# Kernel optimization log

Hardware: AMD Instinct MI355X
Metric: run time of the kernel (lower is better)

The kernel has to match this reference:

```python
import jax, jax.numpy as jnp
import numpy as np

B, N, D, H, DH = 2, 2048, 1024, 16, 64
SCALE = DH ** -0.5


def setup_inputs() -> dict:
    key = jax.random.key(0)
    k1, k2, k3 = jax.random.split(key, 3)
    x = jax.random.normal(k1, (B, N, D), dtype=jnp.float32)
    w_qkv = jax.random.normal(k2, (D, 3 * H * DH), dtype=jnp.float32) * 0.02
    w_out = jax.random.normal(k3, (H * DH, D), dtype=jnp.float32) * 0.02
    # causal boolean mask, broadcast over (b, h)
    attn_mask = jnp.tril(jnp.ones((N, N), dtype=bool))
    return {"x": x, "attn_mask": attn_mask, "w_qkv": w_qkv, "w_out": w_out}


def reference(x, attn_mask, w_qkv, w_out):
    b, n, _ = x.shape
    # fused QKV projection; Rearrange 'b n (qkv h d) -> qkv b h n d'
    qkv = (x @ w_qkv).reshape(b, n, 3, H, DH)
    qkv = jnp.transpose(qkv, (2, 0, 3, 1, 4))  # [3, b, h, n, d]
    q, k, v = qkv[0], qkv[1], qkv[2]
    q = q * SCALE
    sim = jnp.einsum('bhid,bhjd->bhij', q, k)  # [b, h, n, n]
    neg = -jnp.finfo(sim.dtype).max
    sim = jnp.where(attn_mask, sim, neg)
    attn = jax.nn.softmax(sim, axis=-1)
    out = jnp.einsum('bhij,bhjd->bhid', attn, v)  # [b, h, n, d]
    out = jnp.transpose(out, (0, 2, 1, 3)).reshape(b, n, H * DH)
    return out @ w_out
```

## Files before the change

### kernel.cpp

```cpp
#include <hip/hip_runtime.h>
#include <hip/hip_bf16.h>


typedef unsigned short u16;
typedef unsigned int u32;
typedef __bf16 bf16x8 __attribute__((ext_vector_type(8)));
typedef float  f32x4  __attribute__((ext_vector_type(4)));
typedef unsigned short u16x4 __attribute__((ext_vector_type(4)));

#define DEV __device__ __forceinline__

DEV float exp2fast(float x) { return __builtin_amdgcn_exp2f(x); }

DEV u16 f2bf(float f) {
  unsigned u = __builtin_bit_cast(unsigned, f);
  return (u16)((u + 0x7FFFu + ((u >> 16) & 1u)) >> 16);
}

DEV u16 f2bf_fast(float f) {
  __bf16 h = (__bf16)f;
  return __builtin_bit_cast(u16, h);
}

DEV f32x4 mfma16(bf16x8 a, bf16x8 b, f32x4 c) {
  return __builtin_amdgcn_mfma_f32_16x16x32_bf16(a, b, c, 0, 0, 0);
}

template <typename T>
DEV void gload16(const T* g, T* l) {
  __builtin_amdgcn_global_load_lds((__attribute__((address_space(1))) void*)g,
                                   (__attribute__((address_space(3))) void*)l, 16, 0, 0);
}


__global__ __launch_bounds__(256) void prep(const float* __restrict__ x,
                                            const float* __restrict__ wq,
                                            const float* __restrict__ wo,
                                            u16* __restrict__ xb,
                                            u16* __restrict__ dq,
                                            u16* __restrict__ dow) {
  __shared__ u16 T[64][72];
  const int tid = threadIdx.x;
  const int id = (int)blockIdx.x;
  if (id < 4096) {
    int idx = (id * 256 + tid) * 4;
    float4 v = *(const float4*)(x + idx);
    u16x4 u = { f2bf(v.x), f2bf(v.y), f2bf(v.z), f2bf(v.w) };
    *(u16x4*)(xb + idx) = u;
    return;
  }
  int wid = id - 4096;
  int bx = wid & 63, by = wid >> 6;
  const float* src; u16* dst; int C, sl;
  if (bx < 48) { src = wq; dst = dq; C = 3072; sl = 1024; }
  else         { bx -= 48; src = wo; dst = dow; C = 1024; sl = 0; }
  const int c0 = bx * 64, r0 = by * 64;
  const int cl = tid & 63;
  const float scale = (c0 + cl < sl) ? 0.125f * 1.4426950408889634f : 1.0f;
#pragma unroll
  for (int i = 0; i < 16; ++i) {
    int r = (tid >> 6) * 16 + i;
    T[cl][r] = f2bf(src[(size_t)(r0 + r) * C + c0 + cl] * scale);
  }
  __syncthreads();
#pragma unroll
  for (int i = 0; i < 16; ++i) {
    int cc = (tid >> 6) * 16 + i;
    dst[(size_t)(c0 + cc) * 1024 + r0 + cl] = T[cc][cl];
  }
}


__global__ __launch_bounds__(256) void gemm_bf16(const u16* __restrict__ A,
                                                 const u16* __restrict__ Bt,
                                                 u16* __restrict__ qk,
                                                 u16* __restrict__ vt,
                                                 int nx, int cpx) {
  __shared__ __align__(16) u16 lA[128 * 64];
  __shared__ __align__(16) u16 lB[128 * 64];
  const int tid = threadIdx.x;
  const int lane = tid & 63, w = tid >> 6;
  const int g = lane >> 4, r16 = lane & 15;
  const int wm = w >> 1, wn = w & 1;
  const int id = (int)blockIdx.x;
  const int newid = (id & 7) * cpx + (id >> 3);
  const int m0 = (newid / nx) * 128, n0 = (newid % nx) * 128;

  const f32x4 z4 = {0.f, 0.f, 0.f, 0.f};
  f32x4 acc[4][4];
#pragma unroll
  for (int m = 0; m < 4; ++m)
#pragma unroll
    for (int n = 0; n < 4; ++n) acc[m][n] = z4;

  for (int kt = 0; kt < 16; ++kt) {
    const int kbase = kt * 64;
#pragma unroll
    for (int issue = 0; issue < 4; ++issue) {
      int i = issue * 256 + tid;
      int r = i >> 3, jp = (i & 7) ^ (r & 7);
      gload16(A + (size_t)(m0 + r) * 1024 + kbase + jp * 8,
              lA + (size_t)(issue * 256 + (tid & ~63)) * 8);
      gload16(Bt + (size_t)(n0 + r) * 1024 + kbase + jp * 8,
              lB + (size_t)(issue * 256 + (tid & ~63)) * 8);
    }
    __syncthreads();
#pragma unroll
    for (int kk = 0; kk < 2; ++kk) {
      bf16x8 a[4], b[4];
#pragma unroll
      for (int m = 0; m < 4; ++m) {
        int row = wm * 64 + m * 16 + r16;
        int off = row * 128 + ((kk * 64 + g * 16) ^ ((r16 & 7) << 4));
        a[m] = *(const bf16x8*)((const char*)lA + off);
      }
#pragma unroll
      for (int n = 0; n < 4; ++n) {
        int row = wn * 64 + n * 16 + r16;
        int off = row * 128 + ((kk * 64 + g * 16) ^ ((r16 & 7) << 4));
        b[n] = *(const bf16x8*)((const char*)lB + off);
      }
      __builtin_amdgcn_s_setprio(1);
#pragma unroll
      for (int m = 0; m < 4; ++m)
#pragma unroll
        for (int n = 0; n < 4; ++n) acc[m][n] = mfma16(a[m], b[n], acc[m][n]);
      __builtin_amdgcn_s_setprio(0);
    }
    __syncthreads();
  }
  if (n0 < 2048) {
#pragma unroll
    for (int m = 0; m < 4; ++m)
#pragma unroll
      for (int n = 0; n < 4; ++n) {
        int col = n0 + wn * 64 + n * 16 + r16;
#pragma unroll
        for (int j = 0; j < 4; ++j) {
          int row = m0 + wm * 64 + m * 16 + g * 4 + j;
          qk[(size_t)row * 2048 + col] = f2bf(acc[m][n][j]);
        }
      }
  } else {
#pragma unroll
    for (int m = 0; m < 4; ++m) {
      int row0 = m0 + wm * 64 + m * 16 + g * 4;
      int b = row0 >> 11, nn0 = row0 & 2047;
#pragma unroll
      for (int n = 0; n < 4; ++n) {
        int hcol = n0 - 2048 + wn * 64 + n * 16 + r16;
        int h = hcol >> 6, d = hcol & 63;
        u16x4 pk = { f2bf(acc[m][n][0]), f2bf(acc[m][n][1]),
                     f2bf(acc[m][n][2]), f2bf(acc[m][n][3]) };
        *(u16x4*)(vt + (size_t)((b * 16 + h) * 64 + d) * 2048 + nn0) = pk;
      }
    }
  }
}


__global__ __launch_bounds__(256) void gemm64(const u16* __restrict__ A,
                                              const u16* __restrict__ Bt,
                                              float* __restrict__ Cf,
                                              int N, int nx, int cpx) {
  __shared__ __align__(16) u16 lA[64 * 64];
  __shared__ __align__(16) u16 lB[64 * 64];
  const int tid = threadIdx.x;
  const int lane = tid & 63, w = tid >> 6;
  const int g = lane >> 4, r16 = lane & 15;
  const int wm = w >> 1, wn = w & 1;
  const int id = (int)blockIdx.x;
  const int newid = (id & 7) * cpx + (id >> 3);
  const int m0 = (newid / nx) * 64, n0 = (newid % nx) * 64;

  const f32x4 z4 = {0.f, 0.f, 0.f, 0.f};
  f32x4 acc[2][2];
#pragma unroll
  for (int m = 0; m < 2; ++m)
#pragma unroll
    for (int n = 0; n < 2; ++n) acc[m][n] = z4;

  for (int kt = 0; kt < 16; ++kt) {
    const int kbase = kt * 64;
#pragma unroll
    for (int issue = 0; issue < 2; ++issue) {
      int i = issue * 256 + tid;
      int r = i >> 3, jp = (i & 7) ^ (r & 7);
      gload16(A + (size_t)(m0 + r) * 1024 + kbase + jp * 8,
              lA + (size_t)(issue * 256 + (tid & ~63)) * 8);
      gload16(Bt + (size_t)(n0 + r) * 1024 + kbase + jp * 8,
              lB + (size_t)(issue * 256 + (tid & ~63)) * 8);
    }
    __syncthreads();
#pragma unroll
    for (int kk = 0; kk < 2; ++kk) {
      bf16x8 a[2], b[2];
#pragma unroll
      for (int m = 0; m < 2; ++m) {
        int row = wm * 32 + m * 16 + r16;
        int off = row * 128 + ((kk * 64 + g * 16) ^ ((r16 & 7) << 4));
        a[m] = *(const bf16x8*)((const char*)lA + off);
      }
#pragma unroll
      for (int n = 0; n < 2; ++n) {
        int row = wn * 32 + n * 16 + r16;
        int off = row * 128 + ((kk * 64 + g * 16) ^ ((r16 & 7) << 4));
        b[n] = *(const bf16x8*)((const char*)lB + off);
      }
      __builtin_amdgcn_s_setprio(1);
#pragma unroll
      for (int m = 0; m < 2; ++m)
#pragma unroll
        for (int n = 0; n < 2; ++n) acc[m][n] = mfma16(a[m], b[n], acc[m][n]);
      __builtin_amdgcn_s_setprio(0);
    }
    __syncthreads();
  }
#pragma unroll
  for (int m = 0; m < 2; ++m)
#pragma unroll
    for (int n = 0; n < 2; ++n) {
      int col = n0 + wn * 32 + n * 16 + r16;
#pragma unroll
      for (int j = 0; j < 4; ++j) {
        int row = m0 + wm * 32 + m * 16 + g * 4 + j;
        Cf[(size_t)row * N + col] = acc[m][n][j];
      }
    }
}


__global__ __launch_bounds__(256) void attn_fused(const u16* __restrict__ qk,
                                                  const u16* __restrict__ vt,
                                                  u16* __restrict__ ao) {
  __shared__ __align__(16) u16 lK[2][64 * 64];
  __shared__ __align__(16) u16 lV[2][64 * 64];
  const int tid = threadIdx.x;
  const int lane = tid & 63, w = tid >> 6;
  const int g = lane >> 4, r16 = lane & 15;

  const int flat = (int)blockIdx.x;
  const int xcd = flat & 7;
  const int cu = (flat >> 3) & 31;
  const int round = (flat >> 8) & 3;
  const int grp = xcd * 4 + round;
  const int qt = (round < 2) ? (31 - cu) : cu;
  const int b = grp >> 4, h = grp & 15;
  const int q0w = qt * 64 + w * 16;

  bf16x8 aq[2];
  {
    const u16* qrow = qk + (size_t)(b * 2048 + q0w + r16) * 2048 + h * 64;
    aq[0] = *(const bf16x8*)(qrow + g * 8);
    aq[1] = *(const bf16x8*)(qrow + 32 + g * 8);
  }

  const int r = tid >> 3, jp = (tid & 7) ^ (r & 7);
  const int rp = (r & 0x23) | ((r & 0x0C) << 1) | ((r & 0x10) >> 2);
  const u16* ksrc = qk + (size_t)(b * 2048 + rp) * 2048 + 1024 + h * 64 + jp * 8;
  const u16* vsrc = vt + (size_t)((b * 16 + h) * 64 + r) * 2048 + jp * 8;
  const size_t ldst = (size_t)(tid & ~63) * 8;

  const f32x4 z4 = {0.f, 0.f, 0.f, 0.f};
  f32x4 o[4];
#pragma unroll
  for (int n = 0; n < 4; ++n) o[n] = z4;
  float mrun = -INFINITY, lrun = 0.f;

  gload16(ksrc, lK[0] + ldst);
  gload16(ksrc + (size_t)32 * 2048, lK[0] + 2048 + ldst);
  gload16(vsrc, lV[0] + ldst);
  gload16(vsrc + (size_t)32 * 2048, lV[0] + 2048 + ldst);
  __syncthreads();

  int cur = 0;
  for (int t = 0; t <= qt; ++t) {
    if (t < qt) {
      const u16* kn = ksrc + (size_t)(t + 1) * 64 * 2048;
      const u16* vn = vsrc + (size_t)(t + 1) * 64;
      gload16(kn, lK[cur ^ 1] + ldst);
      gload16(kn + (size_t)32 * 2048, lK[cur ^ 1] + 2048 + ldst);
      gload16(vn, lV[cur ^ 1] + ldst);
      gload16(vn + (size_t)32 * 2048, lV[cur ^ 1] + 2048 + ldst);
    }
    f32x4 s[4];
#pragma unroll
    for (int f = 0; f < 4; ++f) s[f] = z4;
    __builtin_amdgcn_s_setprio(1);
#pragma unroll
    for (int kk = 0; kk < 2; ++kk) {
#pragma unroll
      for (int f = 0; f < 4; ++f) {
        int row = f * 16 + r16;
        int off = row * 128 + ((kk * 64 + g * 16) ^ ((r16 & 7) << 4));
        bf16x8 ak = *(const bf16x8*)((const char*)lK[cur] + off);
        s[f] = mfma16(ak, aq[kk], s[f]);
      }
    }
    __builtin_amdgcn_s_setprio(0);
    if (t == qt) {
      const int qrel = w * 16 + r16;
#pragma unroll
      for (int f = 0; f < 4; ++f)
#pragma unroll
        for (int j = 0; j < 4; ++j) {
          int kvt = (f >> 1) * 32 + g * 8 + (f & 1) * 4 + j;
          if (kvt > qrel) s[f][j] = -3.0e38f;
        }
    }
    float mx = fmaxf(fmaxf(fmaxf(s[0][0], s[0][1]), fmaxf(s[0][2], s[0][3])),
                     fmaxf(fmaxf(s[1][0], s[1][1]), fmaxf(s[1][2], s[1][3])));
    mx = fmaxf(mx, fmaxf(fmaxf(fmaxf(s[2][0], s[2][1]), fmaxf(s[2][2], s[2][3])),
                         fmaxf(fmaxf(s[3][0], s[3][1]), fmaxf(s[3][2], s[3][3]))));
    mx = fmaxf(mx, __shfl_xor(mx, 16));
    mx = fmaxf(mx, __shfl_xor(mx, 32));
    if (!__all(mx - mrun <= 8.0f)) {
      float mnew = fmaxf(mrun, mx);
      float corr = exp2fast(mrun - mnew);
      mrun = mnew;
      lrun *= corr;
      float cj[4];
#pragma unroll
      for (int j = 0; j < 4; ++j) cj[j] = __shfl(corr, g * 4 + j);
#pragma unroll
      for (int n = 0; n < 4; ++n)
#pragma unroll
        for (int j = 0; j < 4; ++j) o[n][j] *= cj[j];
    }
    float sm = 0.f;
#pragma unroll
    for (int f = 0; f < 4; ++f)
#pragma unroll
      for (int j = 0; j < 4; ++j) {
        s[f][j] = exp2fast(s[f][j] - mrun);
        sm += s[f][j];
      }
    lrun += sm;

    bf16x8 ap0, ap1;
#pragma unroll
    for (int j = 0; j < 4; ++j) {
      ap0[j]     = (__bf16)s[0][j];
      ap0[j + 4] = (__bf16)s[1][j];
      ap1[j]     = (__bf16)s[2][j];
      ap1[j + 4] = (__bf16)s[3][j];
    }
    __builtin_amdgcn_s_setprio(1);
#pragma unroll
    for (int n = 0; n < 4; ++n) {
      int row = n * 16 + r16;
      int off0 = row * 128 + ((g * 16) ^ ((r16 & 7) << 4));
      int off1 = row * 128 + ((64 + g * 16) ^ ((r16 & 7) << 4));
      bf16x8 bv0 = *(const bf16x8*)((const char*)lV[cur] + off0);
      o[n] = mfma16(ap0, bv0, o[n]);
      bf16x8 bv1 = *(const bf16x8*)((const char*)lV[cur] + off1);
      o[n] = mfma16(ap1, bv1, o[n]);
    }
    __builtin_amdgcn_s_setprio(0);
    __syncthreads();
    cur ^= 1;
  }
  float lt = lrun;
  lt += __shfl_xor(lt, 16);
  lt += __shfl_xor(lt, 32);
  float lj[4];
#pragma unroll
  for (int j = 0; j < 4; ++j) lj[j] = __shfl(lt, g * 4 + j);
#pragma unroll
  for (int n = 0; n < 4; ++n) {
    int col = h * 64 + n * 16 + r16;
#pragma unroll
    for (int j = 0; j < 4; ++j) {
      int row = b * 2048 + q0w + g * 4 + j;
      ao[(size_t)row * 1024 + col] = f2bf_fast(o[n][j] * (1.f / lj[j]));
    }
  }
}


extern "C" void kernel_launch(void* const* d_in, const int* in_sizes, int n_in,
                              void* d_out, int out_size, void* d_ws, size_t ws_size,
                              hipStream_t stream) {
  const float* x     = (const float*)d_in[0];
  const float* w_qkv = (const float*)d_in[2];
  const float* w_out = (const float*)d_in[3];
  float* out = (float*)d_out;

  u16* ws = (u16*)d_ws;
  u16* x_bf  = ws;
  u16* wqkvT = x_bf + (size_t)4096 * 1024;
  u16* woutT = wqkvT + (size_t)3072 * 1024;
  u16* qk    = woutT + (size_t)1024 * 1024;
  u16* vtb   = qk + (size_t)4096 * 2048;
  u16* ao    = vtb + (size_t)2048 * 2048;

  prep<<<5120, 256, 0, stream>>>(x, w_qkv, w_out, x_bf, wqkvT, woutT);
  gemm_bf16<<<768, 256, 0, stream>>>(x_bf, wqkvT, qk, vtb, 24, 96);
  attn_fused<<<1024, 256, 0, stream>>>(qk, vtb, ao);
  gemm64<<<1024, 256, 0, stream>>>(ao, woutT, out, 1024, 16, 128);
}
```

Measured before the change: 192.8 us.

## Double-buffer LDS tiles in both GEMMs and enlarge output GEMM tile to 128x64

Both the QKV GEMM and the output projection GEMM now keep two LDS buffers and issue the global loads for the next K tile before computing on the current one. This removes one barrier per iteration and hides load latency behind the MFMA work. The output GEMM also moves from 64x64 to 128x64 tiles, launched as 512 blocks instead of 1024, which improves reuse of the B tile. In exchange, LDS per block doubles (64KB for the QKV GEMM), which can cut occupancy, and the output GEMM has fewer blocks to spread across the CUs.

```diff
diff --git a/kernel.cpp b/kernel.cpp
--- a/kernel.cpp
+++ b/kernel.cpp
@@ -76,8 +76,8 @@
                                                  u16* __restrict__ qk,
                                                  u16* __restrict__ vt,
                                                  int nx, int cpx) {
-  __shared__ __align__(16) u16 lA[128 * 64];
-  __shared__ __align__(16) u16 lB[128 * 64];
+  __shared__ __align__(16) u16 lA[2][128 * 64];
+  __shared__ __align__(16) u16 lB[2][128 * 64];
   const int tid = threadIdx.x;
   const int lane = tid & 63, w = tid >> 6;
   const int g = lane >> 4, r16 = lane & 15;
@@ -86,6 +86,13 @@
   const int newid = (id & 7) * cpx + (id >> 3);
   const int m0 = (newid / nx) * 128, n0 = (newid % nx) * 128;
 
+  const int sr[4] = { tid >> 3, (256 + tid) >> 3, (512 + tid) >> 3, (768 + tid) >> 3 };
+  int sjp[4];
+#pragma unroll
+  for (int is = 0; is < 4; ++is) sjp[is] = ((is * 256 + tid) & 7) ^ (sr[is] & 7);
+  const size_t sdst[4] = { (size_t)(tid & ~63) * 8, (size_t)(256 + (tid & ~63)) * 8,
+                           (size_t)(512 + (tid & ~63)) * 8, (size_t)(768 + (tid & ~63)) * 8 };
+
   const f32x4 z4 = {0.f, 0.f, 0.f, 0.f};
   f32x4 acc[4][4];
 #pragma unroll
@@ -93,18 +100,23 @@
 #pragma unroll
     for (int n = 0; n < 4; ++n) acc[m][n] = z4;
 
+#pragma unroll
+  for (int is = 0; is < 4; ++is) {
+    gload16(A + (size_t)(m0 + sr[is]) * 1024 + sjp[is] * 8, lA[0] + sdst[is]);
+    gload16(Bt + (size_t)(n0 + sr[is]) * 1024 + sjp[is] * 8, lB[0] + sdst[is]);
+  }
+  __syncthreads();
+
+  int cur = 0;
   for (int kt = 0; kt < 16; ++kt) {
-    const int kbase = kt * 64;
-#pragma unroll
-    for (int issue = 0; issue < 4; ++issue) {
-      int i = issue * 256 + tid;
-      int r = i >> 3, jp = (i & 7) ^ (r & 7);
-      gload16(A + (size_t)(m0 + r) * 1024 + kbase + jp * 8,
-              lA + (size_t)(issue * 256 + (tid & ~63)) * 8);
-      gload16(Bt + (size_t)(n0 + r) * 1024 + kbase + jp * 8,
-              lB + (size_t)(issue * 256 + (tid & ~63)) * 8);
-    }
-    __syncthreads();
+    if (kt < 15) {
+      const int kb = (kt + 1) * 64;
+#pragma unroll
+      for (int is = 0; is < 4; ++is) {
+        gload16(A + (size_t)(m0 + sr[is]) * 1024 + kb + sjp[is] * 8, lA[cur ^ 1] + sdst[is]);
+        gload16(Bt + (size_t)(n0 + sr[is]) * 1024 + kb + sjp[is] * 8, lB[cur ^ 1] + sdst[is]);
+      }
+    }
 #pragma unroll
     for (int kk = 0; kk < 2; ++kk) {
       bf16x8 a[4], b[4];
@@ -112,13 +124,13 @@
       for (int m = 0; m < 4; ++m) {
         int row = wm * 64 + m * 16 + r16;
         int off = row * 128 + ((kk * 64 + g * 16) ^ ((r16 & 7) << 4));
-        a[m] = *(const bf16x8*)((const char*)lA + off);
+        a[m] = *(const bf16x8*)((const char*)lA[cur] + off);
       }
 #pragma unroll
       for (int n = 0; n < 4; ++n) {
         int row = wn * 64 + n * 16 + r16;
         int off = row * 128 + ((kk * 64 + g * 16) ^ ((r16 & 7) << 4));
-        b[n] = *(const bf16x8*)((const char*)lB + off);
+        b[n] = *(const bf16x8*)((const char*)lB[cur] + off);
       }
       __builtin_amdgcn_s_setprio(1);
 #pragma unroll
@@ -128,6 +140,7 @@
       __builtin_amdgcn_s_setprio(0);
     }
     __syncthreads();
+    cur ^= 1;
   }
   if (n0 < 2048) {
 #pragma unroll
@@ -159,72 +172,87 @@
 }
 
 
-__global__ __launch_bounds__(256) void gemm64(const u16* __restrict__ A,
-                                              const u16* __restrict__ Bt,
-                                              float* __restrict__ Cf,
-                                              int N, int nx, int cpx) {
-  __shared__ __align__(16) u16 lA[64 * 64];
-  __shared__ __align__(16) u16 lB[64 * 64];
+__global__ __launch_bounds__(256) void gemm_out(const u16* __restrict__ A,
+                                                const u16* __restrict__ Bt,
+                                                float* __restrict__ Cf,
+                                                int nx, int cpx) {
+  __shared__ __align__(16) u16 lA[2][128 * 64];
+  __shared__ __align__(16) u16 lB[2][64 * 64];
   const int tid = threadIdx.x;
   const int lane = tid & 63, w = tid >> 6;
   const int g = lane >> 4, r16 = lane & 15;
   const int wm = w >> 1, wn = w & 1;
   const int id = (int)blockIdx.x;
   const int newid = (id & 7) * cpx + (id >> 3);
-  const int m0 = (newid / nx) * 64, n0 = (newid % nx) * 64;
+  const int m0 = (newid / nx) * 128, n0 = (newid % nx) * 64;
+
+  const int sr[4] = { tid >> 3, (256 + tid) >> 3, (512 + tid) >> 3, (768 + tid) >> 3 };
+  int sjp[4];
+#pragma unroll
+  for (int is = 0; is < 4; ++is) sjp[is] = ((is * 256 + tid) & 7) ^ (sr[is] & 7);
+  const size_t sdst[4] = { (size_t)(tid & ~63) * 8, (size_t)(256 + (tid & ~63)) * 8,
+                           (size_t)(512 + (tid & ~63)) * 8, (size_t)(768 + (tid & ~63)) * 8 };
 
   const f32x4 z4 = {0.f, 0.f, 0.f, 0.f};
-  f32x4 acc[2][2];
-#pragma unroll
-  for (int m = 0; m < 2; ++m)
+  f32x4 acc[4][2];
+#pragma unroll
+  for (int m = 0; m < 4; ++m)
 #pragma unroll
     for (int n = 0; n < 2; ++n) acc[m][n] = z4;
 
+#pragma unroll
+  for (int is = 0; is < 4; ++is)
+    gload16(A + (size_t)(m0 + sr[is]) * 1024 + sjp[is] * 8, lA[0] + sdst[is]);
+#pragma unroll
+  for (int is = 0; is < 2; ++is)
+    gload16(Bt + (size_t)(n0 + sr[is]) * 1024 + sjp[is] * 8, lB[0] + sdst[is]);
+  __syncthreads();
+
+  int cur = 0;
   for (int kt = 0; kt < 16; ++kt) {
-    const int kbase = kt * 64;
-#pragma unroll
-    for (int issue = 0; issue < 2; ++issue) {
-      int i = issue * 256 + tid;
-      int r = i >> 3, jp = (i & 7) ^ (r & 7);
-      gload16(A + (size_t)(m0 + r) * 1024 + kbase + jp * 8,
-              lA + (size_t)(issue * 256 + (tid & ~63)) * 8);
-      gload16(Bt + (size_t)(n0 + r) * 1024 + kbase + jp * 8,
-              lB + (size_t)(issue * 256 + (tid & ~63)) * 8);
-    }
-    __syncthreads();
+    if (kt < 15) {
+      const int kb = (kt + 1) * 64;
+#pragma unroll
+      for (int is = 0; is < 4; ++is)
+        gload16(A + (size_t)(m0 + sr[is]) * 1024 + kb + sjp[is] * 8, lA[cur ^ 1] + sdst[is]);
+#pragma unroll
+      for (int is = 0; is < 2; ++is)
+        gload16(Bt + (size_t)(n0 + sr[is]) * 1024 + kb + sjp[is] * 8, lB[cur ^ 1] + sdst[is]);
+    }
 #pragma unroll
     for (int kk = 0; kk < 2; ++kk) {
-      bf16x8 a[2], b[2];
-#pragma unroll
-      for (int m = 0; m < 2; ++m) {
-        int row = wm * 32 + m * 16 + r16;
+      bf16x8 a[4], b[2];
+#pragma unroll
+      for (int m = 0; m < 4; ++m) {
+        int row = wm * 64 + m * 16 + r16;
         int off = row * 128 + ((kk * 64 + g * 16) ^ ((r16 & 7) << 4));
-        a[m] = *(const bf16x8*)((const char*)lA + off);
+        a[m] = *(const bf16x8*)((const char*)lA[cur] + off);
       }
 #pragma unroll
       for (int n = 0; n < 2; ++n) {
         int row = wn * 32 + n * 16 + r16;
         int off = row * 128 + ((kk * 64 + g * 16) ^ ((r16 & 7) << 4));
-        b[n] = *(const bf16x8*)((const char*)lB + off);
+        b[n] = *(const bf16x8*)((const char*)lB[cur] + off);
       }
       __builtin_amdgcn_s_setprio(1);
 #pragma unroll
-      for (int m = 0; m < 2; ++m)
+      for (int m = 0; m < 4; ++m)
 #pragma unroll
         for (int n = 0; n < 2; ++n) acc[m][n] = mfma16(a[m], b[n], acc[m][n]);
       __builtin_amdgcn_s_setprio(0);
     }
     __syncthreads();
-  }
-#pragma unroll
-  for (int m = 0; m < 2; ++m)
+    cur ^= 1;
+  }
+#pragma unroll
+  for (int m = 0; m < 4; ++m)
 #pragma unroll
     for (int n = 0; n < 2; ++n) {
       int col = n0 + wn * 32 + n * 16 + r16;
 #pragma unroll
       for (int j = 0; j < 4; ++j) {
-        int row = m0 + wm * 32 + m * 16 + g * 4 + j;
-        Cf[(size_t)row * N + col] = acc[m][n][j];
+        int row = m0 + wm * 64 + m * 16 + g * 4 + j;
+        Cf[(size_t)row * 1024 + col] = acc[m][n][j];
       }
     }
 }
@@ -397,5 +425,5 @@
   prep<<<5120, 256, 0, stream>>>(x, w_qkv, w_out, x_bf, wqkvT, woutT);
   gemm_bf16<<<768, 256, 0, stream>>>(x_bf, wqkvT, qk, vtb, 24, 96);
   attn_fused<<<1024, 256, 0, stream>>>(qk, vtb, ao);
-  gemm64<<<1024, 256, 0, stream>>>(ao, woutT, out, 1024, 16, 128);
-}
+  gemm_out<<<512, 256, 0, stream>>>(ao, woutT, out, 16, 64);
+}
```

Result: no change. 190.4 us (-1.2%).
